# Optimization experiments

Hardware: AMD Instinct MI355X
Metric: run time of the kernel (lower is better)

The kernel has to match this reference:

```python
import jax, jax.numpy as jnp
import numpy as np

N, NDIM, K, M = 65536, 512, 512, 200


def setup_inputs() -> dict:
    key = jax.random.key(0)
    k1, k2, k3, k4, k5 = jax.random.split(key, 5)
    data = jax.random.normal(k1, (N, NDIM), dtype=jnp.float32)
    # Orthogonal projection A, as in __init__: QR of randn with sign fix
    A0 = np.asarray(jax.random.normal(k2, (NDIM, K), dtype=jnp.float32), dtype=np.float64)
    Q, R = np.linalg.qr(A0)
    A = jnp.asarray(Q * np.sign(np.diag(R)), dtype=jnp.float32)
    # Monotonic knot grids on roughly [-4, 4] with M knots per direction
    span = 8.0 / (M - 1)
    dx = jax.random.uniform(k3, (K, M - 1), minval=0.5 * span, maxval=1.5 * span)
    xx = jnp.concatenate([jnp.full((K, 1), -4.0), -4.0 + jnp.cumsum(dx, axis=1)], axis=1).astype(jnp.float32)
    dy = jax.random.uniform(k4, (K, M - 1), minval=0.5 * span, maxval=1.5 * span)
    yy = jnp.concatenate([jnp.full((K, 1), -4.0), -4.0 + jnp.cumsum(dy, axis=1)], axis=1).astype(jnp.float32)
    delta = jax.random.uniform(k5, (K, M), minval=0.5, maxval=2.0, dtype=jnp.float32)
    return {"data": data, "A": A, "xx": xx, "yy": yy, "delta": delta}


def _rq_spline_forward(x, xx, yy, delta):
    """Monotonic rational-quadratic spline, applied per dimension.
    x: (N, K) values; xx, yy, delta: (K, M) knot positions / values / derivatives.
    Returns (y, log|dy/dx|), both (N, K).
    """
    Mk = xx.shape[1]
    # Per-dimension bin search: idx in [0, Mk]
    idx = jax.vmap(jnp.searchsorted, in_axes=(0, 1))(xx, x).T  # (N, K)
    below = idx == 0
    above = idx == Mk
    b = jnp.clip(idx, 1, Mk - 1) - 1  # interior bin index, (N, K)
    bt = b.T  # (K, N) for take_along_axis on (K, M) tables
    g = lambda t, o: jnp.take_along_axis(t, bt + o, axis=1).T  # -> (N, K)
    xk, xk1 = g(xx, 0), g(xx, 1)
    yk, yk1 = g(yy, 0), g(yy, 1)
    dk, dk1 = g(delta, 0), g(delta, 1)
    dx = xk1 - xk
    dy = yk1 - yk
    s = dy / dx  # bin slope
    xi = jnp.clip((x - xk) / dx, 0.0, 1.0)  # clipped so out-of-range pts stay finite
    xi1 = 1.0 - xi
    denom = s + (dk1 + dk - 2.0 * s) * xi * xi1
    y_in = yk + dy * (s * xi * xi + dk * xi * xi1) / denom
    logd_in = (2.0 * jnp.log(s)
               + jnp.log(dk1 * xi * xi + 2.0 * s * xi * xi1 + dk * xi1 * xi1)
               - 2.0 * jnp.log(denom))
    # Linear extrapolation outside the knot range with endpoint derivatives
    x0, xN_ = xx[:, 0], xx[:, -1]
    y0, yN_ = yy[:, 0], yy[:, -1]
    d0, dN_ = delta[:, 0], delta[:, -1]
    y = jnp.where(below, y0 + d0 * (x - x0),
                  jnp.where(above, yN_ + dN_ * (x - xN_), y_in))
    logd = jnp.where(below, jnp.log(d0),
                     jnp.where(above, jnp.log(dN_), logd_in))
    return y, logd


def reference(data, A, xx, yy, delta):
    data0 = data @ A                    # (N, K) sliced projection
    remaining = data - data0 @ A.T      # component orthogonal to the slices
    y, logd = _rq_spline_forward(data0, xx, yy, delta)
    logj = jnp.sum(logd, axis=1)        # (N,) log-Jacobian
    out = remaining + y @ A.T
    return out, logj
```

## Files before the change

### kernel.cpp

```cpp
#include <hip/hip_runtime.h>

#define N_ROWS 65536
#define DIM 512
#define MKNOTS 200
#define KT 8
#define NCELL 768
#define TILE 256
#define TPB 4
#define NKT (DIM / KT)

typedef _Float16 f16x8 __attribute__((ext_vector_type(8)));
typedef _Float16 f16x4 __attribute__((ext_vector_type(4)));
typedef float f32x4 __attribute__((ext_vector_type(4)));
typedef unsigned int u32x4 __attribute__((ext_vector_type(4)));

__device__ inline void gload16(const void* g, void* l) {
  __builtin_amdgcn_global_load_lds(
      (const __attribute__((address_space(1))) void*)g,
      (__attribute__((address_space(3))) void*)l,
      16, 0, 0);
}

template <bool S3, bool ADDSRC>
__global__ __launch_bounds__(256)
void gemm_k(const _Float16* __restrict__ Ah, const _Float16* __restrict__ Al,
            const _Float16* __restrict__ Bth, const _Float16* __restrict__ Btl,
            const float* __restrict__ addsrc, float* __restrict__ C)
{
  __shared__ alignas(16) _Float16 smem[S3 ? 16384 : 8192];
  _Float16* sAh = smem;
  _Float16* sBh = smem + 4096;
  _Float16* sAl = S3 ? smem + 8192  : smem;
  _Float16* sBl = S3 ? smem + 12288 : smem;

  const int tid  = threadIdx.x;
  const int bm   = blockIdx.x * 128;
  const int bn   = blockIdx.y * 128;
  const int wm   = ((tid >> 6) >> 1) * 64;
  const int wn   = ((tid >> 6) & 1) * 64;
  const int lane = tid & 63;
  const int lm   = lane & 15;
  const int quad = lane >> 4;
  const int sr   = tid >> 2;
  const int sc   = (tid & 3) * 8;

  const _Float16* gAh = Ah  + (size_t)(bm + sr) * DIM + sc;
  const _Float16* gBh = Bth + (size_t)(bn + sr) * DIM + sc;
  const _Float16* gAl = S3 ? (Al  + (size_t)(bm + sr) * DIM + sc) : gAh;
  const _Float16* gBl = S3 ? (Btl + (size_t)(bn + sr) * DIM + sc) : gBh;

  f32x4 acc[4][4] = {};

  for (int k0 = 0; k0 < DIM; k0 += 32) {
    gload16(gAh + k0,               sAh + tid * 8);
    gload16(gAh + k0 + 64 * DIM,    sAh + 2048 + tid * 8);
    gload16(gBh + k0,               sBh + tid * 8);
    gload16(gBh + k0 + 64 * DIM,    sBh + 2048 + tid * 8);
    if constexpr (S3) {
      gload16(gAl + k0,             sAl + tid * 8);
      gload16(gAl + k0 + 64 * DIM,  sAl + 2048 + tid * 8);
      gload16(gBl + k0,             sBl + tid * 8);
      gload16(gBl + k0 + 64 * DIM,  sBl + 2048 + tid * 8);
    }
    __syncthreads();

    f16x8 a_h[4], b_h[4], a_l[4], b_l[4];
    #pragma unroll
    for (int i = 0; i < 4; ++i) {
      a_h[i] = *(const f16x8*)&sAh[(wm + i * 16 + lm) * 32 + quad * 8];
      b_h[i] = *(const f16x8*)&sBh[(wn + i * 16 + lm) * 32 + quad * 8];
      if constexpr (S3) {
        a_l[i] = *(const f16x8*)&sAl[(wm + i * 16 + lm) * 32 + quad * 8];
        b_l[i] = *(const f16x8*)&sBl[(wn + i * 16 + lm) * 32 + quad * 8];
      }
    }
    #pragma unroll
    for (int i = 0; i < 4; ++i)
      #pragma unroll
      for (int j = 0; j < 4; ++j) {
        acc[i][j] = __builtin_amdgcn_mfma_f32_16x16x32_f16(a_h[i], b_h[j], acc[i][j], 0, 0, 0);
        if constexpr (S3) {
          acc[i][j] = __builtin_amdgcn_mfma_f32_16x16x32_f16(a_h[i], b_l[j], acc[i][j], 0, 0, 0);
          acc[i][j] = __builtin_amdgcn_mfma_f32_16x16x32_f16(a_l[i], b_h[j], acc[i][j], 0, 0, 0);
        }
      }
    __syncthreads();
  }

  #pragma unroll
  for (int i = 0; i < 4; ++i)
    #pragma unroll
    for (int j = 0; j < 4; ++j)
      #pragma unroll
      for (int r = 0; r < 4; ++r) {
        const int row = bm + wm + i * 16 + quad * 4 + r;
        const int col = bn + wn + j * 16 + lm;
        const size_t idx = (size_t)row * DIM + col;
        float v = acc[i][j][r];
        if constexpr (ADDSRC) v += addsrc[idx];
        C[idx] = v;
      }
}

__global__ __launch_bounds__(256)
void conv_data_k(const float* __restrict__ in, _Float16* __restrict__ hi,
                 _Float16* __restrict__ lo)
{
  const size_t i = ((size_t)blockIdx.x * 256 + threadIdx.x) * 4;
  const float4 v = *reinterpret_cast<const float4*>(in + i);
  f16x4 h, l;
  h.x = (_Float16)v.x; l.x = (_Float16)(v.x - (float)h.x);
  h.y = (_Float16)v.y; l.y = (_Float16)(v.y - (float)h.y);
  h.z = (_Float16)v.z; l.z = (_Float16)(v.z - (float)h.z);
  h.w = (_Float16)v.w; l.w = (_Float16)(v.w - (float)h.w);
  *reinterpret_cast<f16x4*>(hi + i) = h;
  *reinterpret_cast<f16x4*>(lo + i) = l;
}

__global__ __launch_bounds__(256)
void conv_A_k(const float* __restrict__ A, _Float16* __restrict__ Ah,
              _Float16* __restrict__ Al, _Float16* __restrict__ ATh,
              _Float16* __restrict__ ATl)
{
  const int i = blockIdx.x * 256 + threadIdx.x;
  const int r = i >> 9, c = i & 511;
  const float v = A[i];
  const _Float16 h = (_Float16)v;
  const _Float16 l = (_Float16)(v - (float)h);
  Ah[i] = h; Al[i] = l;
  ATh[c * 512 + r] = h; ATl[c * 512 + r] = l;
}

__global__ __launch_bounds__(256)
void prep_k(const float* __restrict__ xx, const float* __restrict__ yy,
            const float* __restrict__ dd, float4* __restrict__ pkG,
            unsigned char* __restrict__ bucketG)
{
  __shared__ float xr[MKNOTS];
  const int k = blockIdx.x, tid = threadIdx.x;
  if (tid < MKNOTS) xr[tid] = xx[k * MKNOTS + tid];
  __syncthreads();
  if (tid < MKNOTS) {
    const float x0 = xr[tid];
    const float y0 = yy[k * MKNOTS + tid];
    const float d0 = dd[k * MKNOTS + tid];
    float rdx = 0.f;
    if (tid < MKNOTS - 1) rdx = 1.0f / (xr[tid + 1] - x0);
    pkG[k * MKNOTS + tid] = float4{x0, y0, d0, rdx};
  }
  for (int c = tid; c < NCELL; c += 256) {
    const float cl = -4.f + (float)c * 0.015625f;
    int lo = 0, hi = MKNOTS;
    while (lo < hi) { const int mid = (lo + hi) >> 1; if (xr[mid] <= cl) lo = mid + 1; else hi = mid; }
    bucketG[k * NCELL + c] = (unsigned char)lo;
  }
}

__global__ __launch_bounds__(256, 5)
void spline_k(const float* __restrict__ data0, const float4* __restrict__ pkG,
              const unsigned char* __restrict__ bucketG,
              _Float16* __restrict__ zH, float* __restrict__ ppart)
{
  __shared__ float4 pkL[KT * 201];

  const int kBase = blockIdx.x * KT;
  const int nBase = blockIdx.y * (TILE * TPB);
  const int tid = threadIdx.x;

  for (int i = tid; i < KT * MKNOTS; i += 256) {
    const int r = i / MKNOTS, c = i - r * MKNOTS;
    pkL[r * 201 + c] = pkG[(kBase + r) * MKNOTS + c];
  }
  if (tid < KT) pkL[tid * 201 + 200] = float4{0.f, 0.f, 0.f, 0.f};
  __syncthreads();

  const unsigned char* bRow = bucketG + (size_t)kBase * NCELL;
  const float* xp0 = data0 + (size_t)(nBase + tid) * DIM + kBase;

  float4 v0 = *(const float4*)xp0;
  float4 v1 = *(const float4*)(xp0 + 4);

  #pragma unroll
  for (int t = 0; t < TPB; ++t) {
    const float x8[8] = {v0.x, v0.y, v0.z, v0.w, v1.x, v1.y, v1.z, v1.w};
    if (t + 1 < TPB) {
      const float* xp = xp0 + (size_t)(t + 1) * TILE * DIM;
      v0 = *(const float4*)xp;
      v1 = *(const float4*)(xp + 4);
    }

    float acc = 0.f;
    float zprev = 0.f;
    unsigned int zw[4];
    #pragma unroll
    for (int j = 0; j < KT; ++j) {
      const float x = x8[j];

      int c = (int)(x * 64.f + 256.f);
      c = min(max(c, 0), NCELL - 1);
      const int cnt = (int)bRow[j * NCELL + c];
      const int q = min(cnt, MKNOTS - 1);
      const float xq = pkL[j * 201 + q].x;
      const int b = min(cnt + (xq < x ? 1 : 0), MKNOTS) - 1;

      const float4 p0 = pkL[j * 201 + b];
      const float4 p1 = pkL[j * 201 + b + 1];

      const float dy = p1.y - p0.y;
      const float s  = dy * p0.w;
      float xi = (x - p0.x) * p0.w;
      xi = fminf(fmaxf(xi, 0.f), 1.f);
      const float xi1 = 1.f - xi;
      const float g = xi * xi1;
      const float den = s + (p1.z + p0.z - 2.f * s) * g;
      const float rden = __builtin_amdgcn_rcpf(den);
      const float y_in = p0.y + dy * (s * xi * xi + p0.z * g) * rden;
      const float dnum = p1.z * xi * xi + 2.f * s * g + p0.z * xi1 * xi1;

      const bool edge = (x <= -4.f) || (b == MKNOTS - 1);
      const float larg = edge ? p0.z : (s * s * dnum) * (rden * rden);
      acc += __logf(larg);
      const float y = edge ? (p0.y + p0.z * (x - p0.x)) : y_in;

      const float z = y - x;
      if (j & 1) {
        union { _Float16 h[2]; unsigned int u; } pk2;
        pk2.h[0] = (_Float16)zprev; pk2.h[1] = (_Float16)z;
        zw[j >> 1] = pk2.u;
      } else {
        zprev = z;
      }
    }

    const int row = nBase + t * TILE + tid;
    ppart[(size_t)blockIdx.x * N_ROWS + row] = acc;
    union { unsigned int w[4]; u32x4 v4; } zu;
    zu.w[0] = zw[0]; zu.w[1] = zw[1]; zu.w[2] = zw[2]; zu.w[3] = zw[3];
    *(u32x4*)(zH + (size_t)row * DIM + kBase) = zu.v4;
  }
}

__global__ __launch_bounds__(256)
void reduce_k(const float* __restrict__ ppart, float* __restrict__ logj)
{
  const int n = blockIdx.x * 256 + threadIdx.x;
  float a = 0.f;
  #pragma unroll
  for (int t = 0; t < NKT; ++t) a += ppart[(size_t)t * N_ROWS + n];
  logj[n] = a;
}

extern "C" void kernel_launch(void* const* d_in, const int* in_sizes, int n_in,
                              void* d_out, int out_size, void* d_ws, size_t ws_size,
                              hipStream_t stream)
{
  const float* data  = (const float*)d_in[0];
  const float* A     = (const float*)d_in[1];
  const float* xx    = (const float*)d_in[2];
  const float* yy    = (const float*)d_in[3];
  const float* delta = (const float*)d_in[4];

  float* out  = (float*)d_out;
  float* logj = out + (size_t)N_ROWS * DIM;

  _Float16* dHi = (_Float16*)d_ws;
  _Float16* dLo = dHi + (size_t)N_ROWS * DIM;
  _Float16* Ah  = dLo + (size_t)N_ROWS * DIM;
  _Float16* Al  = Ah + 512 * 512;
  _Float16* ATh = Al + 512 * 512;
  _Float16* ATl = ATh + 512 * 512;
  float* data0  = (float*)(ATl + 512 * 512);
  _Float16* zH  = dHi;
  float4* pkG = (float4*)dLo;
  unsigned char* bucketG = (unsigned char*)(pkG + 512 * MKNOTS);
  float* ppart = (float*)(bucketG + 512 * NCELL);

  conv_A_k<<<1024, 256, 0, stream>>>(A, Ah, Al, ATh, ATl);
  conv_data_k<<<(N_ROWS * DIM) / (256 * 4), 256, 0, stream>>>(data, dHi, dLo);

  gemm_k<true, false><<<dim3(N_ROWS / 128, DIM / 128), 256, 0, stream>>>(
      dHi, dLo, ATh, ATl, nullptr, data0);

  prep_k<<<512, 256, 0, stream>>>(xx, yy, delta, pkG, bucketG);

  spline_k<<<dim3(DIM / KT, N_ROWS / (TILE * TPB)), 256, 0, stream>>>(
      data0, pkG, bucketG, zH, ppart);

  reduce_k<<<N_ROWS / 256, 256, 0, stream>>>(ppart, logj);

  gemm_k<false, true><<<dim3(N_ROWS / 128, DIM / 128), 256, 0, stream>>>(
      zH, nullptr, Ah, nullptr, data, out);
}
```

Baseline: 665.3 us.

## Widen spline tile to 16 dims with SoA knot tables and fp16 derivatives

Doubles the number of projected dimensions each spline block handles, from 8 to 16, so every thread loads 64 contiguous bytes per row and writes two 16-byte fp16 chunks. The LDS knot table changes from an array of float4 structs to separate x, y and fp16 derivative arrays, and the per-bin reciprocal is now computed in the kernel instead of being precomputed. This keeps LDS use reasonable at the larger tile and aims for wider, better-coalesced memory traffic. In exchange it adds a reciprocal per element, loses precision by storing derivatives in fp16, and lowers the occupancy hint from 5 to 4.

```diff
diff --git a/kernel.cpp b/kernel.cpp
--- a/kernel.cpp
+++ b/kernel.cpp
@@ -3,7 +3,7 @@
 #define N_ROWS 65536
 #define DIM 512
 #define MKNOTS 200
-#define KT 8
+#define KT 16
 #define NCELL 768
 #define TILE 256
 #define TPB 4
@@ -144,9 +144,7 @@
     const float x0 = xr[tid];
     const float y0 = yy[k * MKNOTS + tid];
     const float d0 = dd[k * MKNOTS + tid];
-    float rdx = 0.f;
-    if (tid < MKNOTS - 1) rdx = 1.0f / (xr[tid + 1] - x0);
-    pkG[k * MKNOTS + tid] = float4{x0, y0, d0, rdx};
+    pkG[k * MKNOTS + tid] = float4{x0, y0, d0, 0.f};
   }
   for (int c = tid; c < NCELL; c += 256) {
     const float cl = -4.f + (float)c * 0.015625f;
@@ -156,12 +154,14 @@
   }
 }
 
-__global__ __launch_bounds__(256, 5)
+__global__ __launch_bounds__(256, 4)
 void spline_k(const float* __restrict__ data0, const float4* __restrict__ pkG,
               const unsigned char* __restrict__ bucketG,
               _Float16* __restrict__ zH, float* __restrict__ ppart)
 {
-  __shared__ float4 pkL[KT * 201];
+  __shared__ float sX[KT * 201 + 1];
+  __shared__ float sY[KT * 201 + 1];
+  __shared__ _Float16 sD[KT * 201 + 2];
 
   const int kBase = blockIdx.x * KT;
   const int nBase = blockIdx.y * (TILE * TPB);
@@ -169,9 +169,16 @@
 
   for (int i = tid; i < KT * MKNOTS; i += 256) {
     const int r = i / MKNOTS, c = i - r * MKNOTS;
-    pkL[r * 201 + c] = pkG[(kBase + r) * MKNOTS + c];
-  }
-  if (tid < KT) pkL[tid * 201 + 200] = float4{0.f, 0.f, 0.f, 0.f};
+    const float4 v = pkG[(kBase + r) * MKNOTS + c];
+    sX[r * 201 + c] = v.x;
+    sY[r * 201 + c] = v.y;
+    sD[r * 201 + c] = (_Float16)v.z;
+  }
+  if (tid < KT) {
+    sX[tid * 201 + 200] = 1e30f;
+    sY[tid * 201 + 200] = 0.f;
+    sD[tid * 201 + 200] = (_Float16)1.f;
+  }
   __syncthreads();
 
   const unsigned char* bRow = bucketG + (size_t)kBase * NCELL;
@@ -179,48 +186,58 @@
 
   float4 v0 = *(const float4*)xp0;
   float4 v1 = *(const float4*)(xp0 + 4);
+  float4 v2 = *(const float4*)(xp0 + 8);
+  float4 v3 = *(const float4*)(xp0 + 12);
 
   #pragma unroll
   for (int t = 0; t < TPB; ++t) {
-    const float x8[8] = {v0.x, v0.y, v0.z, v0.w, v1.x, v1.y, v1.z, v1.w};
+    const float x16[16] = {v0.x, v0.y, v0.z, v0.w, v1.x, v1.y, v1.z, v1.w,
+                           v2.x, v2.y, v2.z, v2.w, v3.x, v3.y, v3.z, v3.w};
     if (t + 1 < TPB) {
       const float* xp = xp0 + (size_t)(t + 1) * TILE * DIM;
       v0 = *(const float4*)xp;
       v1 = *(const float4*)(xp + 4);
+      v2 = *(const float4*)(xp + 8);
+      v3 = *(const float4*)(xp + 12);
     }
 
     float acc = 0.f;
     float zprev = 0.f;
-    unsigned int zw[4];
+    unsigned int zw[8];
     #pragma unroll
     for (int j = 0; j < KT; ++j) {
-      const float x = x8[j];
+      const float x = x16[j];
 
       int c = (int)(x * 64.f + 256.f);
       c = min(max(c, 0), NCELL - 1);
       const int cnt = (int)bRow[j * NCELL + c];
       const int q = min(cnt, MKNOTS - 1);
-      const float xq = pkL[j * 201 + q].x;
+      const float xq = sX[j * 201 + q];
       const int b = min(cnt + (xq < x ? 1 : 0), MKNOTS) - 1;
 
-      const float4 p0 = pkL[j * 201 + b];
-      const float4 p1 = pkL[j * 201 + b + 1];
-
-      const float dy = p1.y - p0.y;
-      const float s  = dy * p0.w;
-      float xi = (x - p0.x) * p0.w;
+      const float xk  = sX[j * 201 + b];
+      const float xk1 = sX[j * 201 + b + 1];
+      const float yk  = sY[j * 201 + b];
+      const float yk1 = sY[j * 201 + b + 1];
+      const float dk  = (float)sD[j * 201 + b];
+      const float dk1 = (float)sD[j * 201 + b + 1];
+
+      const float rdx = __builtin_amdgcn_rcpf(xk1 - xk);
+      const float dy  = yk1 - yk;
+      const float s   = dy * rdx;
+      float xi = (x - xk) * rdx;
       xi = fminf(fmaxf(xi, 0.f), 1.f);
       const float xi1 = 1.f - xi;
       const float g = xi * xi1;
-      const float den = s + (p1.z + p0.z - 2.f * s) * g;
+      const float den = s + (dk1 + dk - 2.f * s) * g;
       const float rden = __builtin_amdgcn_rcpf(den);
-      const float y_in = p0.y + dy * (s * xi * xi + p0.z * g) * rden;
-      const float dnum = p1.z * xi * xi + 2.f * s * g + p0.z * xi1 * xi1;
+      const float y_in = yk + dy * (s * xi * xi + dk * g) * rden;
+      const float dnum = dk1 * xi * xi + 2.f * s * g + dk * xi1 * xi1;
 
       const bool edge = (x <= -4.f) || (b == MKNOTS - 1);
-      const float larg = edge ? p0.z : (s * s * dnum) * (rden * rden);
+      const float larg = edge ? dk : (s * s * dnum) * (rden * rden);
       acc += __logf(larg);
-      const float y = edge ? (p0.y + p0.z * (x - p0.x)) : y_in;
+      const float y = edge ? (yk + dk * (x - xk)) : y_in;
 
       const float z = y - x;
       if (j & 1) {
@@ -234,9 +251,12 @@
 
     const int row = nBase + t * TILE + tid;
     ppart[(size_t)blockIdx.x * N_ROWS + row] = acc;
-    union { unsigned int w[4]; u32x4 v4; } zu;
-    zu.w[0] = zw[0]; zu.w[1] = zw[1]; zu.w[2] = zw[2]; zu.w[3] = zw[3];
-    *(u32x4*)(zH + (size_t)row * DIM + kBase) = zu.v4;
+    union { unsigned int w[4]; u32x4 v4; } za, zb;
+    za.w[0] = zw[0]; za.w[1] = zw[1]; za.w[2] = zw[2]; za.w[3] = zw[3];
+    zb.w[0] = zw[4]; zb.w[1] = zw[5]; zb.w[2] = zw[6]; zb.w[3] = zw[7];
+    u32x4* dst = (u32x4*)(zH + (size_t)row * DIM + kBase);
+    dst[0] = za.v4;
+    dst[1] = zb.v4;
   }
 }
 
```

New measurement: 814.8 us. 1.22x slower.

## Produce transposed projection and restructure spline kernel with packed fp16 derivatives

Applied to the files above, without the earlier changes.

The first GEMM now swaps its operands to write data0 transposed (K-major), so the spline kernel reads each dimension's values coalesced across threads. The spline tile grows to 16 dimensions, and the knot table is split into float2 x/y plus fp16-packed (d_k, d_{k+1}) pairs, with the reciprocal bin width computed on the fly instead of stored. z outputs are staged through LDS so that global writes are coalesced. The aims are better memory coalescing and less LDS traffic, at the cost of extra barriers, lower occupancy (launch bounds go from 5 to 3), and reduced precision for the derivatives.

```diff
diff --git a/kernel.cpp b/kernel.cpp
--- a/kernel.cpp
+++ b/kernel.cpp
@@ -3,16 +3,14 @@
 #define N_ROWS 65536
 #define DIM 512
 #define MKNOTS 200
-#define KT 8
+#define KT 16
 #define NCELL 768
-#define TILE 256
 #define TPB 4
 #define NKT (DIM / KT)
 
 typedef _Float16 f16x8 __attribute__((ext_vector_type(8)));
 typedef _Float16 f16x4 __attribute__((ext_vector_type(4)));
 typedef float f32x4 __attribute__((ext_vector_type(4)));
-typedef unsigned int u32x4 __attribute__((ext_vector_type(4)));
 
 __device__ inline void gload16(const void* g, void* l) {
   __builtin_amdgcn_global_load_lds(
@@ -25,7 +23,8 @@
 __global__ __launch_bounds__(256)
 void gemm_k(const _Float16* __restrict__ Ah, const _Float16* __restrict__ Al,
             const _Float16* __restrict__ Bth, const _Float16* __restrict__ Btl,
-            const float* __restrict__ addsrc, float* __restrict__ C)
+            const float* __restrict__ addsrc, float* __restrict__ C,
+            const int ldC)
 {
   __shared__ alignas(16) _Float16 smem[S3 ? 16384 : 8192];
   _Float16* sAh = smem;
@@ -95,7 +94,7 @@
       for (int r = 0; r < 4; ++r) {
         const int row = bm + wm + i * 16 + quad * 4 + r;
         const int col = bn + wn + j * 16 + lm;
-        const size_t idx = (size_t)row * DIM + col;
+        const size_t idx = (size_t)row * ldC + col;
         float v = acc[i][j][r];
         if constexpr (ADDSRC) v += addsrc[idx];
         C[idx] = v;
@@ -144,9 +143,8 @@
     const float x0 = xr[tid];
     const float y0 = yy[k * MKNOTS + tid];
     const float d0 = dd[k * MKNOTS + tid];
-    float rdx = 0.f;
-    if (tid < MKNOTS - 1) rdx = 1.0f / (xr[tid + 1] - x0);
-    pkG[k * MKNOTS + tid] = float4{x0, y0, d0, rdx};
+    const float d1 = (tid < MKNOTS - 1) ? dd[k * MKNOTS + tid + 1] : 1.f;
+    pkG[k * MKNOTS + tid] = float4{x0, y0, d0, d1};
   }
   for (int c = tid; c < NCELL; c += 256) {
     const float cl = -4.f + (float)c * 0.015625f;
@@ -156,71 +154,87 @@
   }
 }
 
-__global__ __launch_bounds__(256, 5)
-void spline_k(const float* __restrict__ data0, const float4* __restrict__ pkG,
+__global__ __launch_bounds__(256, 3)
+void spline_k(const float* __restrict__ data0T, const float4* __restrict__ pkG,
               const unsigned char* __restrict__ bucketG,
               _Float16* __restrict__ zH, float* __restrict__ ppart)
 {
-  __shared__ float4 pkL[KT * 201];
+  __shared__ float2 sXY[KT * 201];
+  __shared__ unsigned int sDD[KT * 201];
+  __shared__ unsigned int zS[256 * 9];
 
   const int kBase = blockIdx.x * KT;
-  const int nBase = blockIdx.y * (TILE * TPB);
+  const int nBase = blockIdx.y * (256 * TPB);
   const int tid = threadIdx.x;
 
   for (int i = tid; i < KT * MKNOTS; i += 256) {
     const int r = i / MKNOTS, c = i - r * MKNOTS;
-    pkL[r * 201 + c] = pkG[(kBase + r) * MKNOTS + c];
-  }
-  if (tid < KT) pkL[tid * 201 + 200] = float4{0.f, 0.f, 0.f, 0.f};
+    const float4 v = pkG[(kBase + r) * MKNOTS + c];
+    sXY[r * 201 + c] = float2{v.x, v.y};
+    union { _Float16 h[2]; unsigned int u; } dp;
+    dp.h[0] = (_Float16)v.z; dp.h[1] = (_Float16)v.w;
+    sDD[r * 201 + c] = dp.u;
+  }
+  if (tid < KT) {
+    sXY[tid * 201 + 200] = float2{1e30f, 0.f};
+    union { _Float16 h[2]; unsigned int u; } dp;
+    dp.h[0] = (_Float16)1.f; dp.h[1] = (_Float16)1.f;
+    sDD[tid * 201 + 200] = dp.u;
+  }
   __syncthreads();
 
   const unsigned char* bRow = bucketG + (size_t)kBase * NCELL;
-  const float* xp0 = data0 + (size_t)(nBase + tid) * DIM + kBase;
-
-  float4 v0 = *(const float4*)xp0;
-  float4 v1 = *(const float4*)(xp0 + 4);
-
+
+  float xc[KT], xn[KT];
   #pragma unroll
+  for (int j = 0; j < KT; ++j)
+    xc[j] = data0T[((size_t)(kBase + j) << 16) + nBase + tid];
+
   for (int t = 0; t < TPB; ++t) {
-    const float x8[8] = {v0.x, v0.y, v0.z, v0.w, v1.x, v1.y, v1.z, v1.w};
+    const int n = nBase + t * 256 + tid;
     if (t + 1 < TPB) {
-      const float* xp = xp0 + (size_t)(t + 1) * TILE * DIM;
-      v0 = *(const float4*)xp;
-      v1 = *(const float4*)(xp + 4);
+      #pragma unroll
+      for (int j = 0; j < KT; ++j)
+        xn[j] = data0T[((size_t)(kBase + j) << 16) + n + 256];
     }
 
     float acc = 0.f;
     float zprev = 0.f;
-    unsigned int zw[4];
+    unsigned int zw[8];
     #pragma unroll
     for (int j = 0; j < KT; ++j) {
-      const float x = x8[j];
+      const float x = xc[j];
 
       int c = (int)(x * 64.f + 256.f);
       c = min(max(c, 0), NCELL - 1);
       const int cnt = (int)bRow[j * NCELL + c];
       const int q = min(cnt, MKNOTS - 1);
-      const float xq = pkL[j * 201 + q].x;
+      const float xq = sXY[j * 201 + q].x;
       const int b = min(cnt + (xq < x ? 1 : 0), MKNOTS) - 1;
 
-      const float4 p0 = pkL[j * 201 + b];
-      const float4 p1 = pkL[j * 201 + b + 1];
-
-      const float dy = p1.y - p0.y;
-      const float s  = dy * p0.w;
-      float xi = (x - p0.x) * p0.w;
+      const float2 p0 = sXY[j * 201 + b];
+      const float2 p1 = sXY[j * 201 + b + 1];
+      union { unsigned int u; _Float16 h[2]; } dp;
+      dp.u = sDD[j * 201 + b];
+      const float dk  = (float)dp.h[0];
+      const float dk1 = (float)dp.h[1];
+
+      const float rdx = __builtin_amdgcn_rcpf(p1.x - p0.x);
+      const float dy  = p1.y - p0.y;
+      const float s   = dy * rdx;
+      float xi = (x - p0.x) * rdx;
       xi = fminf(fmaxf(xi, 0.f), 1.f);
       const float xi1 = 1.f - xi;
       const float g = xi * xi1;
-      const float den = s + (p1.z + p0.z - 2.f * s) * g;
+      const float den = s + (dk1 + dk - 2.f * s) * g;
       const float rden = __builtin_amdgcn_rcpf(den);
-      const float y_in = p0.y + dy * (s * xi * xi + p0.z * g) * rden;
-      const float dnum = p1.z * xi * xi + 2.f * s * g + p0.z * xi1 * xi1;
+      const float y_in = p0.y + dy * (s * xi * xi + dk * g) * rden;
+      const float dnum = dk1 * xi * xi + 2.f * s * g + dk * xi1 * xi1;
 
       const bool edge = (x <= -4.f) || (b == MKNOTS - 1);
-      const float larg = edge ? p0.z : (s * s * dnum) * (rden * rden);
+      const float larg = edge ? dk : (s * s * dnum) * (rden * rden);
       acc += __logf(larg);
-      const float y = edge ? (p0.y + p0.z * (x - p0.x)) : y_in;
+      const float y = edge ? (p0.y + dk * (x - p0.x)) : y_in;
 
       const float z = y - x;
       if (j & 1) {
@@ -231,12 +245,23 @@
         zprev = z;
       }
     }
-
-    const int row = nBase + t * TILE + tid;
-    ppart[(size_t)blockIdx.x * N_ROWS + row] = acc;
-    union { unsigned int w[4]; u32x4 v4; } zu;
-    zu.w[0] = zw[0]; zu.w[1] = zw[1]; zu.w[2] = zw[2]; zu.w[3] = zw[3];
-    *(u32x4*)(zH + (size_t)row * DIM + kBase) = zu.v4;
+    #pragma unroll
+    for (int j = 0; j < KT; ++j) xc[j] = xn[j];
+
+    ppart[(size_t)blockIdx.x * N_ROWS + n] = acc;
+
+    __syncthreads();
+    #pragma unroll
+    for (int w = 0; w < 8; ++w) zS[tid * 9 + w] = zw[w];
+    __syncthreads();
+
+    const int w = tid & 7;
+    #pragma unroll
+    for (int ri = 0; ri < 8; ++ri) {
+      const int r = ri * 32 + (tid >> 3);
+      *(unsigned int*)(zH + (size_t)(nBase + t * 256 + r) * DIM + kBase + w * 2)
+          = zS[r * 9 + w];
+    }
   }
 }
 
@@ -269,7 +294,7 @@
   _Float16* Al  = Ah + 512 * 512;
   _Float16* ATh = Al + 512 * 512;
   _Float16* ATl = ATh + 512 * 512;
-  float* data0  = (float*)(ATl + 512 * 512);
+  float* data0T = (float*)(ATl + 512 * 512);
   _Float16* zH  = dHi;
   float4* pkG = (float4*)dLo;
   unsigned char* bucketG = (unsigned char*)(pkG + 512 * MKNOTS);
@@ -278,16 +303,16 @@
   conv_A_k<<<1024, 256, 0, stream>>>(A, Ah, Al, ATh, ATl);
   conv_data_k<<<(N_ROWS * DIM) / (256 * 4), 256, 0, stream>>>(data, dHi, dLo);
 
-  gemm_k<true, false><<<dim3(N_ROWS / 128, DIM / 128), 256, 0, stream>>>(
-      dHi, dLo, ATh, ATl, nullptr, data0);
+  gemm_k<true, false><<<dim3(DIM / 128, N_ROWS / 128), 256, 0, stream>>>(
+      ATh, ATl, dHi, dLo, nullptr, data0T, N_ROWS);
 
   prep_k<<<512, 256, 0, stream>>>(xx, yy, delta, pkG, bucketG);
 
-  spline_k<<<dim3(DIM / KT, N_ROWS / (TILE * TPB)), 256, 0, stream>>>(
-      data0, pkG, bucketG, zH, ppart);
+  spline_k<<<dim3(DIM / KT, N_ROWS / (256 * TPB)), 256, 0, stream>>>(
+      data0T, pkG, bucketG, zH, ppart);
 
   reduce_k<<<N_ROWS / 256, 256, 0, stream>>>(ppart, logj);
 
   gemm_k<false, true><<<dim3(N_ROWS / 128, DIM / 128), 256, 0, stream>>>(
-      zH, nullptr, Ah, nullptr, data, out);
-}
+      zH, nullptr, Ah, nullptr, data, out, DIM);
+}
```

Measured after the change: 689.6 us. 3.7% more time.
